# Performance work log

Hardware: AMD Instinct MI355X
Metric: run time of the kernel (lower is better)

The kernel has to match this reference:

```python
import jax, jax.numpy as jnp
import numpy as np

N, C, D, H, W = 1, 32, 64, 192, 160


def affine_grid_3d(theta, size):
    # PyTorch F.affine_grid 3D, align_corners=True convention.
    n, c, d, h, w = size
    z = jnp.linspace(-1.0, 1.0, d)
    y = jnp.linspace(-1.0, 1.0, h)
    x = jnp.linspace(-1.0, 1.0, w)
    zz, yy, xx = jnp.meshgrid(z, y, x, indexing='ij')          # [D,H,W]
    base = jnp.stack([xx, yy, zz, jnp.ones_like(xx)], axis=-1)  # [D,H,W,4]
    return jnp.einsum('dhwk,nck->ndhwc', base, theta)           # [N,D,H,W,3] (x,y,z)


def _gather_corner(vol, zi, yi, xi):
    # vol: [C,D,H,W]; zi/yi/xi: [D,H,W] int32. Zero padding outside.
    c, d, h, w = vol.shape
    valid = (zi >= 0) & (zi < d) & (yi >= 0) & (yi < h) & (xi >= 0) & (xi < w)
    zc = jnp.clip(zi, 0, d - 1)
    yc = jnp.clip(yi, 0, h - 1)
    xc = jnp.clip(xi, 0, w - 1)
    flat = vol.reshape(c, d * h * w)
    idx = (zc * h + yc) * w + xc
    vals = jnp.take(flat, idx.reshape(-1), axis=1).reshape(c, *zi.shape)
    return vals * valid[None].astype(vol.dtype)


def grid_sample_3d(inp, grid):
    # Trilinear grid_sample, zeros padding, align_corners=True.
    n, c, d, h, w = inp.shape
    x = (grid[..., 0] + 1.0) * 0.5 * (w - 1)
    y = (grid[..., 1] + 1.0) * 0.5 * (h - 1)
    z = (grid[..., 2] + 1.0) * 0.5 * (d - 1)
    x0 = jnp.floor(x).astype(jnp.int32); x1 = x0 + 1
    y0 = jnp.floor(y).astype(jnp.int32); y1 = y0 + 1
    z0 = jnp.floor(z).astype(jnp.int32); z1 = z0 + 1
    wx = (x - x0.astype(x.dtype))
    wy = (y - y0.astype(y.dtype))
    wz = (z - z0.astype(z.dtype))

    def sample_one(vol, z0, z1, y0, y1, x0, x1, wz, wy, wx):
        out = jnp.zeros((vol.shape[0],) + wz.shape, dtype=vol.dtype)
        for zi, wzc in ((z0, 1.0 - wz), (z1, wz)):
            for yi, wyc in ((y0, 1.0 - wy), (y1, wy)):
                for xi, wxc in ((x0, 1.0 - wx), (x1, wx)):
                    out = out + _gather_corner(vol, zi, yi, xi) * (wzc * wyc * wxc)[None]
        return out

    return jax.vmap(sample_one)(inp, z0, z1, y0, y1, x0, x1, wz, wy, wx)


def setup_inputs() -> dict:
    key = jax.random.key(0)
    k1, k2 = jax.random.split(key)
    inp = jax.random.normal(k1, (N, C, D, H, W), dtype=jnp.float32)
    identity = jnp.asarray([1, 0, 0, 0, 0, 1, 0, 0, 0, 0, 1, 0], dtype=jnp.float32)
    theta = identity + 0.1 * jax.random.normal(k2, (12,), dtype=jnp.float32)
    return {"input": inp, "theta": theta}


def reference(input, theta):
    th = theta.reshape(1, 3, 4)
    grid = affine_grid_3d(th, input.shape)       # [N,D,H,W,3]
    out = grid_sample_3d(input, grid)            # [N,C,D,H,W]
    return jnp.transpose(out, (0, 4, 3, 1, 2))   # [N,W,H,C,D]
```

## Files before the change

kernel.cpp:

```cpp
#include <hip/hip_runtime.h>

constexpr int W_ = 160;
constexpr int H_ = 192;
constexpr int D_ = 64;
constexpr int C_ = 32;
constexpr int HW_ = H_ * W_;
constexpr int DHW = D_ * H_ * W_;
constexpr int CD  = C_ * D_;

typedef float f4_t __attribute__((ext_vector_type(4)));

__global__ void __launch_bounds__(256, 4)
affine_grid_sample_kernel(const float* __restrict__ inp,
                          const float* __restrict__ th,
                          float* __restrict__ out)
{
    __shared__ float lds[2][64 * 65];

    const int t    = threadIdx.x;
    const int lane = t & 63;
    const int sub  = t >> 6;

    const int bid = blockIdx.x;
    const int xcd = bid & 7;
    int local = bid >> 3;
    const int cs = local & 7;
    local >>= 3;
    const int wt = local % 3;
    const int r  = local / 3;
    const int hsub = r & 1;
    const int dt = r >> 1;
    const int h0 = xcd * 24 + hsub * 12;
    const int w0 = wt << 6;
    const int d0 = dt << 4;
    const int c0 = cs << 2;
    const int w  = w0 + lane;

    const float th0 = th[0], th1 = th[1], th2  = th[2],  th3  = th[3];
    const float th4 = th[4], th5 = th[5], th6  = th[6],  th7  = th[7];
    const float th8 = th[8], th9 = th[9], th10 = th[10], th11 = th[11];

    const float xx = fmaf((float)w, 2.0f / (W_ - 1), -1.0f);
    const unsigned mask = (w < W_) ? 0xFFFFFFFFu : 0u;

    const float* __restrict__ base = inp + (size_t)c0 * DHW;

    int buf = 0;
    #pragma unroll 1
    for (int hl = 0; hl < 12; ++hl) {
        const int h = h0 + hl;
        const float yy = fmaf((float)h, 2.0f / (H_ - 1), -1.0f);
        float* __restrict__ L = lds[buf];

        #pragma unroll
        for (int k = 0; k < 4; ++k) {
            const int d = d0 + (sub << 2) + k;
            const float zz = fmaf((float)d, 2.0f / (D_ - 1), -1.0f);
            const float gx = fmaf(th0, xx, fmaf(th1, yy, fmaf(th2,  zz, th3)));
            const float gy = fmaf(th4, xx, fmaf(th5, yy, fmaf(th6,  zz, th7)));
            const float gz = fmaf(th8, xx, fmaf(th9, yy, fmaf(th10, zz, th11)));
            const float px = (gx + 1.0f) * (0.5f * (W_ - 1));
            const float py = (gy + 1.0f) * (0.5f * (H_ - 1));
            const float pz = (gz + 1.0f) * (0.5f * (D_ - 1));
            const float fx = floorf(px), fy = floorf(py), fz = floorf(pz);
            const int ix0 = (int)fx, iy0 = (int)fy, iz0 = (int)fz;
            const int ix1 = ix0 + 1, iy1 = iy0 + 1, iz1 = iz0 + 1;
            const float wx = px - fx, wy = py - fy, wz = pz - fz;
            const float u0 = (ix0 >= 0 && ix0 < W_) ? (1.0f - wx) : 0.0f;
            const float u1 = (ix1 >= 0 && ix1 < W_) ? wx          : 0.0f;
            const float v0 = (iy0 >= 0 && iy0 < H_) ? (1.0f - wy) : 0.0f;
            const float v1 = (iy1 >= 0 && iy1 < H_) ? wy          : 0.0f;
            const float s0 = (iz0 >= 0 && iz0 < D_) ? (1.0f - wz) : 0.0f;
            const float s1 = (iz1 >= 0 && iz1 < D_) ? wz          : 0.0f;
            const int cx0 = min(max(ix0, 0), W_ - 1), cx1 = min(max(ix1, 0), W_ - 1);
            const int cy0 = min(max(iy0, 0), H_ - 1), cy1 = min(max(iy1, 0), H_ - 1);
            const int cz0 = min(max(iz0, 0), D_ - 1), cz1 = min(max(iz1, 0), D_ - 1);
            const unsigned o00 = (unsigned)(cz0 * HW_ + cy0 * W_);
            const unsigned o01 = (unsigned)(cz0 * HW_ + cy1 * W_);
            const unsigned o10 = (unsigned)(cz1 * HW_ + cy0 * W_);
            const unsigned o11 = (unsigned)(cz1 * HW_ + cy1 * W_);
            unsigned o[8];
            o[0] = (o00 + (unsigned)cx0) & mask;
            o[1] = (o00 + (unsigned)cx1) & mask;
            o[2] = (o01 + (unsigned)cx0) & mask;
            o[3] = (o01 + (unsigned)cx1) & mask;
            o[4] = (o10 + (unsigned)cx0) & mask;
            o[5] = (o10 + (unsigned)cx1) & mask;
            o[6] = (o11 + (unsigned)cx0) & mask;
            o[7] = (o11 + (unsigned)cx1) & mask;

            float b[4][8];
            #pragma unroll
            for (int c = 0; c < 4; ++c) {
                const float* __restrict__ pc = base + (size_t)c * DHW;
                #pragma unroll
                for (int j = 0; j < 8; ++j)
                    b[c][j] = pc[o[j]];
            }

            const int ldsb = lane * 65 + ((sub << 2) + k) * 4;
            #pragma unroll
            for (int c = 0; c < 4; ++c) {
                const float r00 = u0 * b[c][0] + u1 * b[c][1];
                const float r01 = u0 * b[c][2] + u1 * b[c][3];
                const float r10 = u0 * b[c][4] + u1 * b[c][5];
                const float r11 = u0 * b[c][6] + u1 * b[c][7];
                const float rz0 = v0 * r00 + v1 * r01;
                const float rz1 = v0 * r10 + v1 * r11;
                L[ldsb + c] = s0 * rz0 + s1 * rz1;
            }
        }
        __syncthreads();

        {
            const int w2 = t >> 2;
            const int q  = t & 3;
            if (w0 + w2 < W_) {
                const int rb = w2 * 65 + q * 16;
                float* ob = out + ((size_t)(w0 + w2) * H_ + h) * CD
                                + (size_t)c0 * D_ + d0 + (q << 2);
                #pragma unroll
                for (int c = 0; c < 4; ++c) {
                    f4_t v;
                    v.x = L[rb + 0  + c];
                    v.y = L[rb + 4  + c];
                    v.z = L[rb + 8  + c];
                    v.w = L[rb + 12 + c];
                    __builtin_nontemporal_store(v, (f4_t*)(ob + (size_t)c * D_));
                }
            }
        }
        buf ^= 1;
    }
}

extern "C" void kernel_launch(void* const* d_in, const int* in_sizes, int n_in,
                              void* d_out, int out_size, void* d_ws, size_t ws_size,
                              hipStream_t stream)
{
    const float* inp = (const float*)d_in[0];
    const float* th  = (const float*)d_in[1];
    float* out = (float*)d_out;

    hipLaunchKernelGGL(affine_grid_sample_kernel, dim3(1536), dim3(256), 0, stream,
                       inp, th, out);
}
```

Baseline: 743.9 us.

## Stage affine-mapped input bounding box in LDS and sample trilinearly from shared memory

```diff
diff --git a/kernel.cpp b/kernel.cpp
--- a/kernel.cpp
+++ b/kernel.cpp
@@ -4,133 +4,187 @@
 constexpr int H_ = 192;
 constexpr int D_ = 64;
 constexpr int C_ = 32;
-constexpr int HW_ = H_ * W_;
-constexpr int DHW = D_ * H_ * W_;
-constexpr int CD  = C_ * D_;
-
-typedef float f4_t __attribute__((ext_vector_type(4)));
-
-__global__ void __launch_bounds__(256, 4)
+constexpr int HW_  = H_ * W_;
+constexpr int DHWi = D_ * HW_;
+constexpr int CD   = C_ * D_;
+
+constexpr int TW = 32, TH = 12, TD = 16;
+constexpr int NWT = W_ / TW;
+constexpr int NHT = H_ / TH;
+constexpr int NDT = D_ / TD;
+constexpr int SPATIAL = NWT * NHT * NDT;
+constexpr int LDSF = 20480;
+
+__global__ void __launch_bounds__(256, 2)
 affine_grid_sample_kernel(const float* __restrict__ inp,
                           const float* __restrict__ th,
                           float* __restrict__ out)
 {
-    __shared__ float lds[2][64 * 65];
-
-    const int t    = threadIdx.x;
-    const int lane = t & 63;
-    const int sub  = t >> 6;
-
-    const int bid = blockIdx.x;
-    const int xcd = bid & 7;
-    int local = bid >> 3;
-    const int cs = local & 7;
-    local >>= 3;
-    const int wt = local % 3;
-    const int r  = local / 3;
-    const int hsub = r & 1;
-    const int dt = r >> 1;
-    const int h0 = xcd * 24 + hsub * 12;
-    const int w0 = wt << 6;
-    const int d0 = dt << 4;
-    const int c0 = cs << 2;
-    const int w  = w0 + lane;
-
-    const float th0 = th[0], th1 = th[1], th2  = th[2],  th3  = th[3];
-    const float th4 = th[4], th5 = th[5], th6  = th[6],  th7  = th[7];
-    const float th8 = th[8], th9 = th[9], th10 = th[10], th11 = th[11];
-
-    const float xx = fmaf((float)w, 2.0f / (W_ - 1), -1.0f);
-    const unsigned mask = (w < W_) ? 0xFFFFFFFFu : 0u;
-
-    const float* __restrict__ base = inp + (size_t)c0 * DHW;
-
-    int buf = 0;
-    #pragma unroll 1
-    for (int hl = 0; hl < 12; ++hl) {
-        const int h = h0 + hl;
-        const float yy = fmaf((float)h, 2.0f / (H_ - 1), -1.0f);
-        float* __restrict__ L = lds[buf];
-
+    __shared__ float Lb[LDSF];
+
+    const int t = threadIdx.x;
+
+    int bid = blockIdx.x;
+    const int c = bid / SPATIAL;
+    int sp = bid - c * SPATIAL;
+    const int wt = sp % NWT; sp /= NWT;
+    const int hs = sp % NHT;
+    const int dt = sp / NHT;
+    const int w0 = wt * TW, h0 = hs * TH, d0 = dt * TD;
+
+    const float th0=th[0], th1=th[1], th2 =th[2],  th3 =th[3];
+    const float th4=th[4], th5=th[5], th6 =th[6],  th7 =th[7];
+    const float th8=th[8], th9=th[9], th10=th[10], th11=th[11];
+
+    const float* __restrict__ pc = inp + (size_t)c * DHWi;
+
+    auto XX = [&](int w){ return fmaf((float)w, 2.0f/(W_-1), -1.0f); };
+    auto YY = [&](int h){ return fmaf((float)h, 2.0f/(H_-1), -1.0f); };
+    auto ZZ = [&](int d){ return fmaf((float)d, 2.0f/(D_-1), -1.0f); };
+    auto PX = [&](float xx, float yy, float zz){
+        return (fmaf(th0, xx, fmaf(th1, yy, fmaf(th2, zz, th3))) + 1.0f) * (0.5f*(W_-1)); };
+    auto PY = [&](float xx, float yy, float zz){
+        return (fmaf(th4, xx, fmaf(th5, yy, fmaf(th6, zz, th7))) + 1.0f) * (0.5f*(H_-1)); };
+    auto PZ = [&](float xx, float yy, float zz){
+        return (fmaf(th8, xx, fmaf(th9, yy, fmaf(th10, zz, th11))) + 1.0f) * (0.5f*(D_-1)); };
+
+    struct Box { int xlo, ylo, zlo, BX, BY, BZ; bool fits; };
+    auto make_box = [&](int wa, int wspan) -> Box {
+        float pxmn= 1e30f, pxmx=-1e30f, pymn= 1e30f, pymx=-1e30f,
+              pzmn= 1e30f, pzmx=-1e30f;
         #pragma unroll
-        for (int k = 0; k < 4; ++k) {
-            const int d = d0 + (sub << 2) + k;
-            const float zz = fmaf((float)d, 2.0f / (D_ - 1), -1.0f);
-            const float gx = fmaf(th0, xx, fmaf(th1, yy, fmaf(th2,  zz, th3)));
-            const float gy = fmaf(th4, xx, fmaf(th5, yy, fmaf(th6,  zz, th7)));
-            const float gz = fmaf(th8, xx, fmaf(th9, yy, fmaf(th10, zz, th11)));
-            const float px = (gx + 1.0f) * (0.5f * (W_ - 1));
-            const float py = (gy + 1.0f) * (0.5f * (H_ - 1));
-            const float pz = (gz + 1.0f) * (0.5f * (D_ - 1));
-            const float fx = floorf(px), fy = floorf(py), fz = floorf(pz);
-            const int ix0 = (int)fx, iy0 = (int)fy, iz0 = (int)fz;
-            const int ix1 = ix0 + 1, iy1 = iy0 + 1, iz1 = iz0 + 1;
-            const float wx = px - fx, wy = py - fy, wz = pz - fz;
-            const float u0 = (ix0 >= 0 && ix0 < W_) ? (1.0f - wx) : 0.0f;
-            const float u1 = (ix1 >= 0 && ix1 < W_) ? wx          : 0.0f;
-            const float v0 = (iy0 >= 0 && iy0 < H_) ? (1.0f - wy) : 0.0f;
-            const float v1 = (iy1 >= 0 && iy1 < H_) ? wy          : 0.0f;
-            const float s0 = (iz0 >= 0 && iz0 < D_) ? (1.0f - wz) : 0.0f;
-            const float s1 = (iz1 >= 0 && iz1 < D_) ? wz          : 0.0f;
-            const int cx0 = min(max(ix0, 0), W_ - 1), cx1 = min(max(ix1, 0), W_ - 1);
-            const int cy0 = min(max(iy0, 0), H_ - 1), cy1 = min(max(iy1, 0), H_ - 1);
-            const int cz0 = min(max(iz0, 0), D_ - 1), cz1 = min(max(iz1, 0), D_ - 1);
-            const unsigned o00 = (unsigned)(cz0 * HW_ + cy0 * W_);
-            const unsigned o01 = (unsigned)(cz0 * HW_ + cy1 * W_);
-            const unsigned o10 = (unsigned)(cz1 * HW_ + cy0 * W_);
-            const unsigned o11 = (unsigned)(cz1 * HW_ + cy1 * W_);
-            unsigned o[8];
-            o[0] = (o00 + (unsigned)cx0) & mask;
-            o[1] = (o00 + (unsigned)cx1) & mask;
-            o[2] = (o01 + (unsigned)cx0) & mask;
-            o[3] = (o01 + (unsigned)cx1) & mask;
-            o[4] = (o10 + (unsigned)cx0) & mask;
-            o[5] = (o10 + (unsigned)cx1) & mask;
-            o[6] = (o11 + (unsigned)cx0) & mask;
-            o[7] = (o11 + (unsigned)cx1) & mask;
-
-            float b[4][8];
-            #pragma unroll
-            for (int c = 0; c < 4; ++c) {
-                const float* __restrict__ pc = base + (size_t)c * DHW;
+        for (int ci = 0; ci < 8; ++ci) {
+            const int cw = (ci & 1) ? wa + wspan - 1 : wa;
+            const int ch = (ci & 2) ? h0 + TH - 1    : h0;
+            const int cd = (ci & 4) ? d0 + TD - 1    : d0;
+            const float xx = XX(cw), yy = YY(ch), zz = ZZ(cd);
+            const float px = PX(xx,yy,zz), py = PY(xx,yy,zz), pz = PZ(xx,yy,zz);
+            pxmn = fminf(pxmn, px); pxmx = fmaxf(pxmx, px);
+            pymn = fminf(pymn, py); pymx = fmaxf(pymx, py);
+            pzmn = fminf(pzmn, pz); pzmx = fmaxf(pzmx, pz);
+        }
+        Box b;
+        b.xlo = max((int)floorf(pxmn), 0);
+        int xhi = min((int)floorf(pxmx) + 1, W_ - 1);
+        b.ylo = max((int)floorf(pymn), 0);
+        int yhi = min((int)floorf(pymx) + 1, H_ - 1);
+        b.zlo = max((int)floorf(pzmn), 0);
+        int zhi = min((int)floorf(pzmx) + 1, D_ - 1);
+        b.BX = xhi - b.xlo + 1; if (b.BX < 1) { b.BX = 1; b.xlo = 0; }
+        b.BY = yhi - b.ylo + 1; if (b.BY < 1) { b.BY = 1; b.ylo = 0; }
+        b.BZ = zhi - b.zlo + 1; if (b.BZ < 1) { b.BZ = 1; b.zlo = 0; }
+        const int R = b.BZ * b.BY;
+        b.fits = (b.BX <= 64) && (b.BY <= 128) && (R <= 512) &&
+                 (b.BX * R + 1 <= LDSF);
+        return b;
+    };
+
+    Box full = make_box(w0, TW);
+    const int nsplit = full.fits ? 1 : 2;
+
+    const int dd = t & 15;
+    const int ww = t >> 4;
+
+    for (int s = 0; s < nsplit; ++s) {
+        const int wspan = TW / nsplit;
+        const int wa = w0 + s * wspan;
+        const Box b = (nsplit == 1) ? full : make_box(wa, wspan);
+        const int xlo = b.xlo, ylo = b.ylo, zlo = b.zlo;
+        const int BX = b.BX, BY = b.BY, BZ = b.BZ;
+        const int R = BZ * BY;
+        const bool fits = b.fits;
+
+        if (fits) {
+            const int wv = t >> 6, lane = t & 63;
+            const unsigned m18 = (262144u + (unsigned)BY - 1) / (unsigned)BY;
+            const float* __restrict__ gpz = pc + zlo * HW_ + ylo * W_ + xlo;
+            const bool lx = (lane < BX);
+            for (int rb = wv * 8; rb < R; rb += 32) {
+                float v[8];
                 #pragma unroll
-                for (int j = 0; j < 8; ++j)
-                    b[c][j] = pc[o[j]];
-            }
-
-            const int ldsb = lane * 65 + ((sub << 2) + k) * 4;
-            #pragma unroll
-            for (int c = 0; c < 4; ++c) {
-                const float r00 = u0 * b[c][0] + u1 * b[c][1];
-                const float r01 = u0 * b[c][2] + u1 * b[c][3];
-                const float r10 = u0 * b[c][4] + u1 * b[c][5];
-                const float r11 = u0 * b[c][6] + u1 * b[c][7];
-                const float rz0 = v0 * r00 + v1 * r01;
-                const float rz1 = v0 * r10 + v1 * r11;
-                L[ldsb + c] = s0 * rz0 + s1 * rz1;
+                for (int j = 0; j < 8; ++j) {
+                    const int r  = min(rb + j, R - 1);
+                    const int bz = (int)(((unsigned)r * m18) >> 18);
+                    const int by = r - bz * BY;
+                    v[j] = lx ? gpz[bz * HW_ + by * W_ + lane] : 0.0f;
+                }
+                #pragma unroll
+                for (int j = 0; j < 8; ++j) {
+                    const int r = rb + j;
+                    if (r < R && lx) Lb[r * BX + lane] = v[j];
+                }
             }
         }
         __syncthreads();
 
-        {
-            const int w2 = t >> 2;
-            const int q  = t & 3;
-            if (w0 + w2 < W_) {
-                const int rb = w2 * 65 + q * 16;
-                float* ob = out + ((size_t)(w0 + w2) * H_ + h) * CD
-                                + (size_t)c0 * D_ + d0 + (q << 2);
-                #pragma unroll
-                for (int c = 0; c < 4; ++c) {
-                    f4_t v;
-                    v.x = L[rb + 0  + c];
-                    v.y = L[rb + 4  + c];
-                    v.z = L[rb + 8  + c];
-                    v.w = L[rb + 12 + c];
-                    __builtin_nontemporal_store(v, (f4_t*)(ob + (size_t)c * D_));
+        const int wsteps = wspan >> 4;
+        const int d = d0 + dd;
+        const float kzx = fmaf(th2,  ZZ(d), th3);
+        const float kzy = fmaf(th6,  ZZ(d), th7);
+        const float kzz = fmaf(th10, ZZ(d), th11);
+        for (int wi = 0; wi < wsteps; ++wi) {
+            const int w = wa + wi * 16 + ww;
+            const float xx = XX(w);
+            float* ob = out + ((size_t)w * H_ + h0) * CD + (size_t)c * D_ + d;
+            #pragma unroll 2
+            for (int hh = 0; hh < TH; ++hh) {
+                const float yy = YY(h0 + hh);
+                const float px = (fmaf(th0, xx, fmaf(th1, yy, kzx)) + 1.0f) * (0.5f*(W_-1));
+                const float py = (fmaf(th4, xx, fmaf(th5, yy, kzy)) + 1.0f) * (0.5f*(H_-1));
+                const float pz = (fmaf(th8, xx, fmaf(th9, yy, kzz)) + 1.0f) * (0.5f*(D_-1));
+                const float fx = floorf(px), fy = floorf(py), fz = floorf(pz);
+                const int ix0 = (int)fx, iy0 = (int)fy, iz0 = (int)fz;
+                const float wx = px - fx, wy = py - fy, wz = pz - fz;
+                const float u0r = ((unsigned)ix0     < (unsigned)W_) ? 1.0f - wx : 0.0f;
+                const float u1r = ((unsigned)(ix0+1) < (unsigned)W_) ? wx        : 0.0f;
+                const float v0  = ((unsigned)iy0     < (unsigned)H_) ? 1.0f - wy : 0.0f;
+                const float v1  = ((unsigned)(iy0+1) < (unsigned)H_) ? wy        : 0.0f;
+                const float s0  = ((unsigned)iz0     < (unsigned)D_) ? 1.0f - wz : 0.0f;
+                const float s1  = ((unsigned)(iz0+1) < (unsigned)D_) ? wz        : 0.0f;
+                const int cx0 = min(max(ix0,   0), W_-1);
+                const int cy0 = min(max(iy0,   0), H_-1);
+                const int cy1 = min(max(iy0+1, 0), H_-1);
+                const int cz0 = min(max(iz0,   0), D_-1);
+                const int cz1 = min(max(iz0+1, 0), D_-1);
+                float val;
+                if (__builtin_expect(fits, 1)) {
+                    float u0 = u0r, u1 = u1r;
+                    if (ix0 < 0) { u0 = u1r; u1 = 0.0f; }
+                    const int bx = cx0 - xlo;
+                    const int r00 = (cz0 - zlo) * BY + (cy0 - ylo);
+                    const int r01 = (cz0 - zlo) * BY + (cy1 - ylo);
+                    const int r10 = (cz1 - zlo) * BY + (cy0 - ylo);
+                    const int r11 = (cz1 - zlo) * BY + (cy1 - ylo);
+                    const unsigned cap = (unsigned)(LDSF - 2);
+                    const unsigned i00 = min((unsigned)(r00 * BX + bx), cap);
+                    const unsigned i01 = min((unsigned)(r01 * BX + bx), cap);
+                    const unsigned i10 = min((unsigned)(r10 * BX + bx), cap);
+                    const unsigned i11 = min((unsigned)(r11 * BX + bx), cap);
+                    const float a0 = u0 * Lb[i00] + u1 * Lb[i00 + 1];
+                    const float a1 = u0 * Lb[i01] + u1 * Lb[i01 + 1];
+                    const float a2 = u0 * Lb[i10] + u1 * Lb[i10 + 1];
+                    const float a3 = u0 * Lb[i11] + u1 * Lb[i11 + 1];
+                    const float e0 = v0 * a0 + v1 * a1;
+                    const float e1 = v0 * a2 + v1 * a3;
+                    val = s0 * e0 + s1 * e1;
+                } else {
+                    const int cx1 = min(max(ix0+1, 0), W_-1);
+                    const int g00 = (cz0 * H_ + cy0) * W_;
+                    const int g01 = (cz0 * H_ + cy1) * W_;
+                    const int g10 = (cz1 * H_ + cy0) * W_;
+                    const int g11 = (cz1 * H_ + cy1) * W_;
+                    const float a0 = u0r * pc[g00+cx0] + u1r * pc[g00+cx1];
+                    const float a1 = u0r * pc[g01+cx0] + u1r * pc[g01+cx1];
+                    const float a2 = u0r * pc[g10+cx0] + u1r * pc[g10+cx1];
+                    const float a3 = u0r * pc[g11+cx0] + u1r * pc[g11+cx1];
+                    const float e0 = v0 * a0 + v1 * a1;
+                    const float e1 = v0 * a2 + v1 * a3;
+                    val = s0 * e0 + s1 * e1;
                 }
+                __builtin_nontemporal_store(val, ob + (size_t)hh * CD);
             }
         }
-        buf ^= 1;
+        __syncthreads();
     }
 }
 
@@ -142,6 +196,6 @@
     const float* th  = (const float*)d_in[1];
     float* out = (float*)d_out;
 
-    hipLaunchKernelGGL(affine_grid_sample_kernel, dim3(1536), dim3(256), 0, stream,
-                       inp, th, out);
+    hipLaunchKernelGGL(affine_grid_sample_kernel, dim3(C_ * SPATIAL), dim3(256),
+                       0, stream, inp, th, out);
 }
```

Result: slower. 796.3 us (+7.0%).

## Retile grid-sample to one channel per block with smaller W tiles

Applied to the files above, without the earlier changes.

```diff
diff --git a/kernel.cpp b/kernel.cpp
--- a/kernel.cpp
+++ b/kernel.cpp
@@ -4,74 +4,85 @@
 constexpr int H_ = 192;
 constexpr int D_ = 64;
 constexpr int C_ = 32;
-constexpr int HW_ = H_ * W_;
-constexpr int DHW = D_ * H_ * W_;
-constexpr int CD  = C_ * D_;
+constexpr int HW_  = H_ * W_;
+constexpr int DHWi = D_ * HW_;
+constexpr int CD   = C_ * D_;
+
+constexpr int TW = 32, TH = 12, TD = 16;
+constexpr int NWT = W_ / TW;
+constexpr int NHT = H_ / TH;
+constexpr int NDT = D_ / TD;
+constexpr int QPP = NWT * NHT;
+constexpr int CPX = C_ / 8;
+constexpr int NPH = CPX * NDT;
+constexpr int LDS_BYTES = 53248;
+constexpr int LSTR = 20;
 
 typedef float f4_t __attribute__((ext_vector_type(4)));
+typedef float f2_t __attribute__((ext_vector_type(2)));
 
-__global__ void __launch_bounds__(256, 4)
+__global__ void __launch_bounds__(256)
 affine_grid_sample_kernel(const float* __restrict__ inp,
                           const float* __restrict__ th,
                           float* __restrict__ out)
 {
-    __shared__ float lds[2][64 * 65];
+    extern __shared__ float smem[];
 
-    const int t    = threadIdx.x;
-    const int lane = t & 63;
-    const int sub  = t >> 6;
-
+    const int t   = threadIdx.x;
     const int bid = blockIdx.x;
     const int xcd = bid & 7;
-    int local = bid >> 3;
-    const int cs = local & 7;
-    local >>= 3;
-    const int wt = local % 3;
-    const int r  = local / 3;
-    const int hsub = r & 1;
-    const int dt = r >> 1;
-    const int h0 = xcd * 24 + hsub * 12;
-    const int w0 = wt << 6;
-    const int d0 = dt << 4;
-    const int c0 = cs << 2;
-    const int w  = w0 + lane;
+    int r = bid >> 3;
+    const int phase = r / QPP;
+    const int q     = r - phase * QPP;
+    const int c  = xcd * CPX + (phase >> 2);
+    const int dt = phase & 3;
+    const int hs = q / NWT;
+    const int wt = q - hs * NWT;
+    const int w0 = wt * TW, h0 = hs * TH, d0 = dt * TD;
 
-    const float th0 = th[0], th1 = th[1], th2  = th[2],  th3  = th[3];
-    const float th4 = th[4], th5 = th[5], th6  = th[6],  th7  = th[7];
-    const float th8 = th[8], th9 = th[9], th10 = th[10], th11 = th[11];
+    const float th0=th[0], th1=th[1], th2 =th[2],  th3 =th[3];
+    const float th4=th[4], th5=th[5], th6 =th[6],  th7 =th[7];
+    const float th8=th[8], th9=th[9], th10=th[10], th11=th[11];
 
+    const float* __restrict__ pc = inp + (size_t)c * DHWi;
+
+    const int w = w0 + (t & 31);
+    const int g = t >> 5;
     const float xx = fmaf((float)w, 2.0f / (W_ - 1), -1.0f);
-    const unsigned mask = (w < W_) ? 0xFFFFFFFFu : 0u;
 
-    const float* __restrict__ base = inp + (size_t)c0 * DHW;
+    float kzx[2], kzy[2], kzz[2];
+    #pragma unroll
+    for (int kk = 0; kk < 2; ++kk) {
+        const int d = d0 + 2 * g + kk;
+        const float zz = fmaf((float)d, 2.0f / (D_ - 1), -1.0f);
+        kzx[kk] = fmaf(th2,  zz, th3);
+        kzy[kk] = fmaf(th6,  zz, th7);
+        kzz[kk] = fmaf(th10, zz, th11);
+    }
 
-    int buf = 0;
     #pragma unroll 1
-    for (int hl = 0; hl < 12; ++hl) {
+    for (int hl = 0; hl < TH; ++hl) {
         const int h = h0 + hl;
         const float yy = fmaf((float)h, 2.0f / (H_ - 1), -1.0f);
-        float* __restrict__ L = lds[buf];
+        float* __restrict__ L = smem + (hl & 1) * (TW * LSTR);
 
+        unsigned o[2][8];
+        float u0a[2], u1a[2], v0a[2], v1a[2], s0a[2], s1a[2];
         #pragma unroll
-        for (int k = 0; k < 4; ++k) {
-            const int d = d0 + (sub << 2) + k;
-            const float zz = fmaf((float)d, 2.0f / (D_ - 1), -1.0f);
-            const float gx = fmaf(th0, xx, fmaf(th1, yy, fmaf(th2,  zz, th3)));
-            const float gy = fmaf(th4, xx, fmaf(th5, yy, fmaf(th6,  zz, th7)));
-            const float gz = fmaf(th8, xx, fmaf(th9, yy, fmaf(th10, zz, th11)));
-            const float px = (gx + 1.0f) * (0.5f * (W_ - 1));
-            const float py = (gy + 1.0f) * (0.5f * (H_ - 1));
-            const float pz = (gz + 1.0f) * (0.5f * (D_ - 1));
+        for (int kk = 0; kk < 2; ++kk) {
+            const float px = (fmaf(th0, xx, fmaf(th1, yy, kzx[kk])) + 1.0f) * (0.5f * (W_ - 1));
+            const float py = (fmaf(th4, xx, fmaf(th5, yy, kzy[kk])) + 1.0f) * (0.5f * (H_ - 1));
+            const float pz = (fmaf(th8, xx, fmaf(th9, yy, kzz[kk])) + 1.0f) * (0.5f * (D_ - 1));
             const float fx = floorf(px), fy = floorf(py), fz = floorf(pz);
             const int ix0 = (int)fx, iy0 = (int)fy, iz0 = (int)fz;
             const int ix1 = ix0 + 1, iy1 = iy0 + 1, iz1 = iz0 + 1;
             const float wx = px - fx, wy = py - fy, wz = pz - fz;
-            const float u0 = (ix0 >= 0 && ix0 < W_) ? (1.0f - wx) : 0.0f;
-            const float u1 = (ix1 >= 0 && ix1 < W_) ? wx          : 0.0f;
-            const float v0 = (iy0 >= 0 && iy0 < H_) ? (1.0f - wy) : 0.0f;
-            const float v1 = (iy1 >= 0 && iy1 < H_) ? wy          : 0.0f;
-            const float s0 = (iz0 >= 0 && iz0 < D_) ? (1.0f - wz) : 0.0f;
-            const float s1 = (iz1 >= 0 && iz1 < D_) ? wz          : 0.0f;
+            u0a[kk] = (ix0 >= 0 && ix0 < W_) ? (1.0f - wx) : 0.0f;
+            u1a[kk] = (ix1 >= 0 && ix1 < W_) ? wx          : 0.0f;
+            v0a[kk] = (iy0 >= 0 && iy0 < H_) ? (1.0f - wy) : 0.0f;
+            v1a[kk] = (iy1 >= 0 && iy1 < H_) ? wy          : 0.0f;
+            s0a[kk] = (iz0 >= 0 && iz0 < D_) ? (1.0f - wz) : 0.0f;
+            s1a[kk] = (iz1 >= 0 && iz1 < D_) ? wz          : 0.0f;
             const int cx0 = min(max(ix0, 0), W_ - 1), cx1 = min(max(ix1, 0), W_ - 1);
             const int cy0 = min(max(iy0, 0), H_ - 1), cy1 = min(max(iy1, 0), H_ - 1);
             const int cz0 = min(max(iz0, 0), D_ - 1), cz1 = min(max(iz1, 0), D_ - 1);
@@ -79,58 +90,46 @@
             const unsigned o01 = (unsigned)(cz0 * HW_ + cy1 * W_);
             const unsigned o10 = (unsigned)(cz1 * HW_ + cy0 * W_);
             const unsigned o11 = (unsigned)(cz1 * HW_ + cy1 * W_);
-            unsigned o[8];
-            o[0] = (o00 + (unsigned)cx0) & mask;
-            o[1] = (o00 + (unsigned)cx1) & mask;
-            o[2] = (o01 + (unsigned)cx0) & mask;
-            o[3] = (o01 + (unsigned)cx1) & mask;
-            o[4] = (o10 + (unsigned)cx0) & mask;
-            o[5] = (o10 + (unsigned)cx1) & mask;
-            o[6] = (o11 + (unsigned)cx0) & mask;
-            o[7] = (o11 + (unsigned)cx1) & mask;
+            o[kk][0] = o00 + (unsigned)cx0;
+            o[kk][1] = o00 + (unsigned)cx1;
+            o[kk][2] = o01 + (unsigned)cx0;
+            o[kk][3] = o01 + (unsigned)cx1;
+            o[kk][4] = o10 + (unsigned)cx0;
+            o[kk][5] = o10 + (unsigned)cx1;
+            o[kk][6] = o11 + (unsigned)cx0;
+            o[kk][7] = o11 + (unsigned)cx1;
+        }
 
-            float b[4][8];
+        float b[2][8];
+        #pragma unroll
+        for (int kk = 0; kk < 2; ++kk)
             #pragma unroll
-            for (int c = 0; c < 4; ++c) {
-                const float* __restrict__ pc = base + (size_t)c * DHW;
-                #pragma unroll
-                for (int j = 0; j < 8; ++j)
-                    b[c][j] = pc[o[j]];
-            }
+            for (int j = 0; j < 8; ++j)
+                b[kk][j] = pc[o[kk][j]];
 
-            const int ldsb = lane * 65 + ((sub << 2) + k) * 4;
-            #pragma unroll
-            for (int c = 0; c < 4; ++c) {
-                const float r00 = u0 * b[c][0] + u1 * b[c][1];
-                const float r01 = u0 * b[c][2] + u1 * b[c][3];
-                const float r10 = u0 * b[c][4] + u1 * b[c][5];
-                const float r11 = u0 * b[c][6] + u1 * b[c][7];
-                const float rz0 = v0 * r00 + v1 * r01;
-                const float rz1 = v0 * r10 + v1 * r11;
-                L[ldsb + c] = s0 * rz0 + s1 * rz1;
-            }
+        f2_t val;
+        #pragma unroll
+        for (int kk = 0; kk < 2; ++kk) {
+            const float r00 = u0a[kk] * b[kk][0] + u1a[kk] * b[kk][1];
+            const float r01 = u0a[kk] * b[kk][2] + u1a[kk] * b[kk][3];
+            const float r10 = u0a[kk] * b[kk][4] + u1a[kk] * b[kk][5];
+            const float r11 = u0a[kk] * b[kk][6] + u1a[kk] * b[kk][7];
+            const float e0 = v0a[kk] * r00 + v1a[kk] * r01;
+            const float e1 = v0a[kk] * r10 + v1a[kk] * r11;
+            val[kk] = s0a[kk] * e0 + s1a[kk] * e1;
         }
+        *(f2_t*)&L[(t & 31) * LSTR + 2 * g] = val;
+
         __syncthreads();
 
-        {
+        if (t < 128) {
             const int w2 = t >> 2;
-            const int q  = t & 3;
-            if (w0 + w2 < W_) {
-                const int rb = w2 * 65 + q * 16;
-                float* ob = out + ((size_t)(w0 + w2) * H_ + h) * CD
-                                + (size_t)c0 * D_ + d0 + (q << 2);
-                #pragma unroll
-                for (int c = 0; c < 4; ++c) {
-                    f4_t v;
-                    v.x = L[rb + 0  + c];
-                    v.y = L[rb + 4  + c];
-                    v.z = L[rb + 8  + c];
-                    v.w = L[rb + 12 + c];
-                    __builtin_nontemporal_store(v, (f4_t*)(ob + (size_t)c * D_));
-                }
-            }
+            const int qd = t & 3;
+            const f4_t v = *(const f4_t*)&L[w2 * LSTR + 4 * qd];
+            float* ob = out + ((size_t)(w0 + w2) * H_ + h) * CD
+                            + (size_t)c * D_ + d0 + 4 * qd;
+            __builtin_nontemporal_store(v, (f4_t*)ob);
         }
-        buf ^= 1;
     }
 }
 
@@ -142,6 +141,6 @@
     const float* th  = (const float*)d_in[1];
     float* out = (float*)d_out;
 
-    hipLaunchKernelGGL(affine_grid_sample_kernel, dim3(1536), dim3(256), 0, stream,
-                       inp, th, out);
+    hipLaunchKernelGGL(affine_grid_sample_kernel, dim3(8 * NPH * QPP), dim3(256),
+                       LDS_BYTES, stream, inp, th, out);
 }
```

Result: faster. 709.1 us (-4.7%).
